# Kernel optimization log

Hardware: AMD Instinct MI355X
Metric: run time of the kernel (lower is better)

Reference implementation:

```python
import jax, jax.numpy as jnp
import numpy as np

B, C, H, W = 8, 128, 64, 64
CQK = C // 8


def setup_inputs() -> dict:
    key = jax.random.key(0)
    ks = jax.random.split(key, 7)
    scale = 1.0 / np.sqrt(C)
    return {
        "x": jax.random.normal(ks[0], (B, C, H, W), dtype=jnp.float32),
        "wq": jax.random.normal(ks[1], (CQK, C), dtype=jnp.float32) * scale,
        "bq": jax.random.normal(ks[2], (CQK,), dtype=jnp.float32) * 0.01,
        "wk": jax.random.normal(ks[3], (CQK, C), dtype=jnp.float32) * scale,
        "bk": jax.random.normal(ks[4], (CQK,), dtype=jnp.float32) * 0.01,
        "wv": jax.random.normal(ks[5], (C, C), dtype=jnp.float32) * scale,
        "bv": jax.random.normal(ks[6], (C,), dtype=jnp.float32) * 0.01,
    }


def reference(x, wq, bq, wk, bk, wv, bv):
    b, c, h, w = x.shape
    n = h * w
    xf = x.reshape(b, c, n)                                  # [B,C,N]
    # 1x1 convs == channel matmuls
    q = jnp.einsum('oc,bcn->bon', wq, xf) + bq[:, None]      # [B,C/8,N]
    k = jnp.einsum('oc,bcn->bon', wk, xf) + bk[:, None]      # [B,C/8,N]
    v = jnp.einsum('oc,bcn->bon', wv, xf) + bv[:, None]      # [B,C,N]
    # energy[b,i,j] = <q[:,i], k[:,j]>  (note: NO 1/sqrt(d) scale, per source)
    energy = jnp.einsum('bci,bcj->bij', q, k)                # [B,N,N]
    att = jax.nn.softmax(energy, axis=-1)                    # softmax over j
    # out[b,c,i] = sum_j v[b,c,j] * att[b,i,j]
    out = jnp.einsum('bcj,bij->bci', v, att).reshape(b, c, h, w)
    return out + x
```

## Files before the change

### kernel.cpp

```cpp
#include <hip/hip_runtime.h>
#include <math.h>

#define NB  8
#define NC  128
#define NN  4096
#define NCQ 16
#define BI  64
#define BJ  64
#define NT  (NN / BJ)
#define WROWS 160

typedef __attribute__((ext_vector_type(8))) short short8v;
typedef __attribute__((ext_vector_type(4))) short short4v;
typedef __attribute__((ext_vector_type(4))) float f32x4;

__device__ __forceinline__ short f2bf(float f) {
    unsigned u = __builtin_bit_cast(unsigned, f);
    u += 0x7fffu + ((u >> 16) & 1u);
    return (short)(u >> 16);
}
__device__ __forceinline__ float bf2f(short h) {
    return __builtin_bit_cast(float, ((unsigned)(unsigned short)h) << 16);
}

__global__ __launch_bounds__(256) void wconv(
    const float* __restrict__ wq, const float* __restrict__ bq,
    const float* __restrict__ wk, const float* __restrict__ bk,
    const float* __restrict__ wv, const float* __restrict__ bv,
    short* __restrict__ whg, short* __restrict__ wlg, float* __restrict__ biasg)
{
    const int idx = blockIdx.x * 256 + threadIdx.x;
    if (idx < WROWS * NC) {
        const int row = idx >> 7, k = idx & 127;
        const float v = (row < 16) ? wq[row * NC + k]
                       : (row < 32) ? wk[(row - 16) * NC + k]
                                    : wv[(row - 32) * NC + k];
        const short h = f2bf(v);
        whg[idx] = h;
        wlg[idx] = f2bf(v - bf2f(h));
    }
    if (idx < WROWS)
        biasg[idx] = (idx < 16) ? bq[idx] : (idx < 32) ? bk[idx - 16] : bv[idx - 32];
}

__global__ __launch_bounds__(256) void qkv_gemm(
    const float* __restrict__ x,
    const short* __restrict__ whg, const short* __restrict__ wlg,
    const float* __restrict__ biasg,
    short* __restrict__ Qo, short* __restrict__ KoT, short* __restrict__ Vo)
{
    __shared__ __align__(16) short xsT[2][64][136];

    const int b  = blockIdx.y;
    const int n0 = blockIdx.x * 64;
    const int t  = threadIdx.x;
    const int w  = t >> 6;
    const int l  = t & 63;
    const int lr = l & 15;
    const int g  = l >> 4;

    const float* xb = x + (size_t)b * NC * NN;

#pragma unroll
    for (int it = 0; it < 8; ++it) {
        const int idx4 = t + 256 * it;
        const int cr = idx4 >> 4;
        const int j4 = (idx4 & 15) * 4;
        const float4 v = *reinterpret_cast<const float4*>(xb + (size_t)cr * NN + n0 + j4);
        const float vf[4] = {v.x, v.y, v.z, v.w};
#pragma unroll
        for (int p = 0; p < 4; ++p) {
            const short h = f2bf(vf[p]);
            xsT[0][j4 + p][cr] = h;
            xsT[1][j4 + p][cr] = f2bf(vf[p] - bf2f(h));
        }
    }
    __syncthreads();

    const int lc = 16 * w + lr;
    f32x4 acc[10];
#pragma unroll
    for (int rt = 0; rt < 10; ++rt) acc[rt] = {0.f, 0.f, 0.f, 0.f};

#pragma unroll
    for (int ks = 0; ks < 4; ++ks) {
        const short8v xh = *reinterpret_cast<const short8v*>(&xsT[0][lc][32 * ks + 8 * g]);
        const short8v xl = *reinterpret_cast<const short8v*>(&xsT[1][lc][32 * ks + 8 * g]);
#pragma unroll
        for (int rt = 0; rt < 10; ++rt) {
            const int wo = (16 * rt + lr) * NC + 32 * ks + 8 * g;
            const short8v ah = *reinterpret_cast<const short8v*>(whg + wo);
            const short8v al = *reinterpret_cast<const short8v*>(wlg + wo);
            acc[rt] = __builtin_amdgcn_mfma_f32_16x16x32_bf16(ah, xh, acc[rt], 0, 0, 0);
            acc[rt] = __builtin_amdgcn_mfma_f32_16x16x32_bf16(ah, xl, acc[rt], 0, 0, 0);
            acc[rt] = __builtin_amdgcn_mfma_f32_16x16x32_bf16(al, xh, acc[rt], 0, 0, 0);
        }
    }

    const int col = n0 + lc;
#pragma unroll
    for (int rt = 0; rt < 10; ++rt) {
#pragma unroll
        for (int r = 0; r < 4; ++r) {
            const int ch = 16 * rt + 4 * g + r;
            const short o = f2bf(acc[rt][r] + biasg[ch]);
            if (rt == 0)
                Qo[((size_t)b * NCQ + ch) * NN + col] = o;
            else if (rt == 1)
                KoT[((size_t)b * NN + col) * NCQ + (ch - 16)] = o;
            else
                Vo[((size_t)b * NC + (ch - 32)) * NN + col] = o;
        }
    }
}

__global__ __launch_bounds__(256) void attn_mfma(
    const short* __restrict__ Q, const short* __restrict__ KT,
    const short* __restrict__ V, const float* __restrict__ x,
    float* __restrict__ out)
{
    __shared__ __align__(16) short psT[2][64][72];
    __shared__ float lsumX[4][4][16];

    const int b  = blockIdx.y;
    const int i0 = blockIdx.x * BI;
    const int t  = threadIdx.x;
    const int w  = t >> 6;
    const int l  = t & 63;
    const int lr = l & 15;
    const int g  = l >> 4;

    const short* Qb  = Q  + (size_t)b * NCQ * NN;
    const short* KTb = KT + (size_t)b * NN * NCQ;
    const short* Vb  = V  + (size_t)b * NC * NN;

    const short8v kzero = {0, 0, 0, 0, 0, 0, 0, 0};
    const f32x4   fzero = {0.f, 0.f, 0.f, 0.f};

    short8v qf[4] = {kzero, kzero, kzero, kzero};
    if (g < 2) {
#pragma unroll
        for (int it = 0; it < 4; ++it) {
            const short* qp = Qb + (size_t)(8 * g) * NN + i0 + 16 * it + lr;
#pragma unroll
            for (int e = 0; e < 8; ++e) qf[it][e] = qp[(size_t)e * NN];
        }
    }

    short8v kfA = kzero;
    if (g < 2)
        kfA = *reinterpret_cast<const short8v*>(KTb + (size_t)(16 * w + lr) * NCQ + 8 * g);

    f32x4 acc[2][4];
#pragma unroll
    for (int ct = 0; ct < 2; ++ct)
#pragma unroll
        for (int it = 0; it < 4; ++it) acc[ct][it] = fzero;
    float lsum[4] = {0.f, 0.f, 0.f, 0.f};

    for (int jt = 0; jt < NT; ++jt) {
        const int cur = jt & 1;

        short8v kfB = kzero;
        if (jt + 1 < NT && g < 2)
            kfB = *reinterpret_cast<const short8v*>(
                    KTb + (size_t)((jt + 1) * BJ + 16 * w + lr) * NCQ + 8 * g);

        short8v vf00, vf01, vf10, vf11;
        if (jt > 0) {
            const short* vp = Vb + (size_t)(32 * w + lr) * NN + (jt - 1) * BJ + 8 * g;
            vf00 = *reinterpret_cast<const short8v*>(vp);
            vf01 = *reinterpret_cast<const short8v*>(vp + 32);
            vf10 = *reinterpret_cast<const short8v*>(vp + 16 * NN);
            vf11 = *reinterpret_cast<const short8v*>(vp + 16 * NN + 32);
        }

        f32x4 e0 = __builtin_amdgcn_mfma_f32_16x16x32_bf16(kfA, qf[0], fzero, 0, 0, 0);
        f32x4 e1 = __builtin_amdgcn_mfma_f32_16x16x32_bf16(kfA, qf[1], fzero, 0, 0, 0);
        f32x4 e2 = __builtin_amdgcn_mfma_f32_16x16x32_bf16(kfA, qf[2], fzero, 0, 0, 0);
        f32x4 e3 = __builtin_amdgcn_mfma_f32_16x16x32_bf16(kfA, qf[3], fzero, 0, 0, 0);

#pragma unroll
        for (int r = 0; r < 4; ++r) e0[r] = __expf(e0[r]);
#pragma unroll
        for (int r = 0; r < 4; ++r) e1[r] = __expf(e1[r]);
#pragma unroll
        for (int r = 0; r < 4; ++r) e2[r] = __expf(e2[r]);
#pragma unroll
        for (int r = 0; r < 4; ++r) e3[r] = __expf(e3[r]);
        lsum[0] += (e0[0] + e0[1]) + (e0[2] + e0[3]);
        lsum[1] += (e1[0] + e1[1]) + (e1[2] + e1[3]);
        lsum[2] += (e2[0] + e2[1]) + (e2[2] + e2[3]);
        lsum[3] += (e3[0] + e3[1]) + (e3[2] + e3[3]);

        if (jt > 0) {
            const int prev = cur ^ 1;
            __builtin_amdgcn_s_setprio(1);
#pragma unroll
            for (int ks = 0; ks < 2; ++ks) {
#pragma unroll
                for (int it = 0; it < 4; ++it) {
                    const short8v pf = *reinterpret_cast<const short8v*>(
                            &psT[prev][16 * it + lr][32 * ks + 8 * g]);
                    acc[0][it] = __builtin_amdgcn_mfma_f32_16x16x32_bf16(
                            ks ? vf01 : vf00, pf, acc[0][it], 0, 0, 0);
                    acc[1][it] = __builtin_amdgcn_mfma_f32_16x16x32_bf16(
                            ks ? vf11 : vf10, pf, acc[1][it], 0, 0, 0);
                }
            }
            __builtin_amdgcn_s_setprio(0);
        }

#define P_STORE(ET, IT)                                                           \
        {                                                                         \
            unsigned p01 = (unsigned short)f2bf(ET[0]) |                          \
                           ((unsigned)(unsigned short)f2bf(ET[1]) << 16);         \
            unsigned p23 = (unsigned short)f2bf(ET[2]) |                          \
                           ((unsigned)(unsigned short)f2bf(ET[3]) << 16);         \
            *reinterpret_cast<unsigned*>(&psT[cur][16 * (IT) + lr][16 * w + 4 * g])     = p01; \
            *reinterpret_cast<unsigned*>(&psT[cur][16 * (IT) + lr][16 * w + 4 * g + 2]) = p23; \
        }
        P_STORE(e0, 0) P_STORE(e1, 1) P_STORE(e2, 2) P_STORE(e3, 3)
#undef P_STORE

        __syncthreads();
        kfA = kfB;
    }

    {
        const int prev = (NT - 1) & 1;
        const short* vp = Vb + (size_t)(32 * w + lr) * NN + (NT - 1) * BJ + 8 * g;
        const short8v vf00 = *reinterpret_cast<const short8v*>(vp);
        const short8v vf01 = *reinterpret_cast<const short8v*>(vp + 32);
        const short8v vf10 = *reinterpret_cast<const short8v*>(vp + 16 * NN);
        const short8v vf11 = *reinterpret_cast<const short8v*>(vp + 16 * NN + 32);
#pragma unroll
        for (int ks = 0; ks < 2; ++ks) {
#pragma unroll
            for (int it = 0; it < 4; ++it) {
                const short8v pf = *reinterpret_cast<const short8v*>(
                        &psT[prev][16 * it + lr][32 * ks + 8 * g]);
                acc[0][it] = __builtin_amdgcn_mfma_f32_16x16x32_bf16(
                        ks ? vf01 : vf00, pf, acc[0][it], 0, 0, 0);
                acc[1][it] = __builtin_amdgcn_mfma_f32_16x16x32_bf16(
                        ks ? vf11 : vf10, pf, acc[1][it], 0, 0, 0);
            }
        }
    }

#pragma unroll
    for (int it = 0; it < 4; ++it) {
        lsum[it] += __shfl_xor(lsum[it], 16);
        lsum[it] += __shfl_xor(lsum[it], 32);
    }
    if (l < 16) {
#pragma unroll
        for (int it = 0; it < 4; ++it) lsumX[w][it][l] = lsum[it];
    }
    __syncthreads();
    float inv[4];
#pragma unroll
    for (int it = 0; it < 4; ++it) {
        const float lr_tot = (lsumX[0][it][lr] + lsumX[1][it][lr]) +
                             (lsumX[2][it][lr] + lsumX[3][it][lr]);
        inv[it] = 1.f / lr_tot;
    }

#pragma unroll
    for (int ct = 0; ct < 2; ++ct) {
#pragma unroll
        for (int it = 0; it < 4; ++it) {
#pragma unroll
            for (int r = 0; r < 4; ++r) {
                const int c = 32 * w + 16 * ct + 4 * g + r;
                const size_t o = ((size_t)b * NC + c) * NN + i0 + 16 * it + lr;
                out[o] = acc[ct][it][r] * inv[it] + x[o];
            }
        }
    }
}

extern "C" void kernel_launch(void* const* d_in, const int* in_sizes, int n_in,
                              void* d_out, int out_size, void* d_ws, size_t ws_size,
                              hipStream_t stream) {
    const float* x  = (const float*)d_in[0];
    const float* wq = (const float*)d_in[1];
    const float* bq = (const float*)d_in[2];
    const float* wk = (const float*)d_in[3];
    const float* bk = (const float*)d_in[4];
    const float* wv = (const float*)d_in[5];
    const float* bv = (const float*)d_in[6];
    float* out = (float*)d_out;

    short* ws = (short*)d_ws;
    short* Qo  = ws;
    short* KoT = ws + (size_t)NB * NCQ * NN;
    short* Vo  = ws + 2 * (size_t)NB * NCQ * NN;
    short* whg = ws + 10 * (size_t)NB * NCQ * NN;
    short* wlg = whg + WROWS * NC;
    float* biasg = (float*)(wlg + WROWS * NC);

    wconv<<<dim3(80), 256, 0, stream>>>(wq, bq, wk, bk, wv, bv, whg, wlg, biasg);
    qkv_gemm<<<dim3(NN / 64, NB), 256, 0, stream>>>(x, whg, wlg, biasg, Qo, KoT, Vo);
    attn_mfma<<<dim3(NN / BI, NB), 256, 0, stream>>>(Qo, KoT, Vo, x, out);
}
```

Baseline: 174.6 us.

## Prefetch V tile one iteration ahead with register ping-pong and packed bf16 convert

The attention loop is unrolled by two, alternating between two register sets for K and V fragments. V for tile jt is now loaded during iteration jt and consumed in jt+1, instead of being loaded right before use, so global-memory latency is hidden behind a full iteration. The manual f2bf rounding is replaced by the v_cvt_pk_bf16_f32 instruction, and the tail PV MFMAs get raised priority. This costs extra VGPRs for the double-buffered V fragments, which may reduce occupancy.

```diff
diff --git a/kernel.cpp b/kernel.cpp
--- a/kernel.cpp
+++ b/kernel.cpp
@@ -147,10 +147,13 @@
         }
     }
 
-    short8v kfA = kzero;
+    short8v kfA = kzero, kfB = kzero;
     if (g < 2)
         kfA = *reinterpret_cast<const short8v*>(KTb + (size_t)(16 * w + lr) * NCQ + 8 * g);
 
+    short8v vfE0 = kzero, vfE1 = kzero, vfE2 = kzero, vfE3 = kzero;
+    short8v vfO0 = kzero, vfO1 = kzero, vfO2 = kzero, vfO3 = kzero;
+
     f32x4 acc[2][4];
 #pragma unroll
     for (int ct = 0; ct < 2; ++ct)
@@ -158,94 +161,91 @@
         for (int it = 0; it < 4; ++it) acc[ct][it] = fzero;
     float lsum[4] = {0.f, 0.f, 0.f, 0.f};
 
-    for (int jt = 0; jt < NT; ++jt) {
-        const int cur = jt & 1;
-
-        short8v kfB = kzero;
-        if (jt + 1 < NT && g < 2)
-            kfB = *reinterpret_cast<const short8v*>(
-                    KTb + (size_t)((jt + 1) * BJ + 16 * w + lr) * NCQ + 8 * g);
-
-        short8v vf00, vf01, vf10, vf11;
-        if (jt > 0) {
-            const short* vp = Vb + (size_t)(32 * w + lr) * NN + (jt - 1) * BJ + 8 * g;
-            vf00 = *reinterpret_cast<const short8v*>(vp);
-            vf01 = *reinterpret_cast<const short8v*>(vp + 32);
-            vf10 = *reinterpret_cast<const short8v*>(vp + 16 * NN);
-            vf11 = *reinterpret_cast<const short8v*>(vp + 16 * NN + 32);
-        }
-
-        f32x4 e0 = __builtin_amdgcn_mfma_f32_16x16x32_bf16(kfA, qf[0], fzero, 0, 0, 0);
-        f32x4 e1 = __builtin_amdgcn_mfma_f32_16x16x32_bf16(kfA, qf[1], fzero, 0, 0, 0);
-        f32x4 e2 = __builtin_amdgcn_mfma_f32_16x16x32_bf16(kfA, qf[2], fzero, 0, 0, 0);
-        f32x4 e3 = __builtin_amdgcn_mfma_f32_16x16x32_bf16(kfA, qf[3], fzero, 0, 0, 0);
-
-#pragma unroll
-        for (int r = 0; r < 4; ++r) e0[r] = __expf(e0[r]);
-#pragma unroll
-        for (int r = 0; r < 4; ++r) e1[r] = __expf(e1[r]);
-#pragma unroll
-        for (int r = 0; r < 4; ++r) e2[r] = __expf(e2[r]);
-#pragma unroll
-        for (int r = 0; r < 4; ++r) e3[r] = __expf(e3[r]);
-        lsum[0] += (e0[0] + e0[1]) + (e0[2] + e0[3]);
-        lsum[1] += (e1[0] + e1[1]) + (e1[2] + e1[3]);
-        lsum[2] += (e2[0] + e2[1]) + (e2[2] + e2[3]);
-        lsum[3] += (e3[0] + e3[1]) + (e3[2] + e3[3]);
-
-        if (jt > 0) {
-            const int prev = cur ^ 1;
-            __builtin_amdgcn_s_setprio(1);
-#pragma unroll
-            for (int ks = 0; ks < 2; ++ks) {
-#pragma unroll
-                for (int it = 0; it < 4; ++it) {
-                    const short8v pf = *reinterpret_cast<const short8v*>(
-                            &psT[prev][16 * it + lr][32 * ks + 8 * g]);
-                    acc[0][it] = __builtin_amdgcn_mfma_f32_16x16x32_bf16(
-                            ks ? vf01 : vf00, pf, acc[0][it], 0, 0, 0);
-                    acc[1][it] = __builtin_amdgcn_mfma_f32_16x16x32_bf16(
-                            ks ? vf11 : vf10, pf, acc[1][it], 0, 0, 0);
-                }
-            }
-            __builtin_amdgcn_s_setprio(0);
-        }
-
-#define P_STORE(ET, IT)                                                           \
+#define ATTN_ITER(JT, CUR, KUSE, KLOAD, VU0, VU1, VU2, VU3, VL0, VL1, VL2, VL3)   \
+    {                                                                             \
+        if ((JT) + 1 < NT && g < 2)                                               \
+            KLOAD = *reinterpret_cast<const short8v*>(                            \
+                    KTb + (size_t)(((JT) + 1) * BJ + 16 * w + lr) * NCQ + 8 * g); \
         {                                                                         \
-            unsigned p01 = (unsigned short)f2bf(ET[0]) |                          \
-                           ((unsigned)(unsigned short)f2bf(ET[1]) << 16);         \
-            unsigned p23 = (unsigned short)f2bf(ET[2]) |                          \
-                           ((unsigned)(unsigned short)f2bf(ET[3]) << 16);         \
-            *reinterpret_cast<unsigned*>(&psT[cur][16 * (IT) + lr][16 * w + 4 * g])     = p01; \
-            *reinterpret_cast<unsigned*>(&psT[cur][16 * (IT) + lr][16 * w + 4 * g + 2]) = p23; \
-        }
-        P_STORE(e0, 0) P_STORE(e1, 1) P_STORE(e2, 2) P_STORE(e3, 3)
-#undef P_STORE
-
-        __syncthreads();
-        kfA = kfB;
-    }
+            const short* vp = Vb + (size_t)(32 * w + lr) * NN + (JT) * BJ + 8 * g;\
+            VL0 = *reinterpret_cast<const short8v*>(vp);                          \
+            VL1 = *reinterpret_cast<const short8v*>(vp + 32);                     \
+            VL2 = *reinterpret_cast<const short8v*>(vp + 16 * NN);                \
+            VL3 = *reinterpret_cast<const short8v*>(vp + 16 * NN + 32);           \
+        }                                                                         \
+        f32x4 e0 = __builtin_amdgcn_mfma_f32_16x16x32_bf16(KUSE, qf[0], fzero, 0, 0, 0); \
+        f32x4 e1 = __builtin_amdgcn_mfma_f32_16x16x32_bf16(KUSE, qf[1], fzero, 0, 0, 0); \
+        f32x4 e2 = __builtin_amdgcn_mfma_f32_16x16x32_bf16(KUSE, qf[2], fzero, 0, 0, 0); \
+        f32x4 e3 = __builtin_amdgcn_mfma_f32_16x16x32_bf16(KUSE, qf[3], fzero, 0, 0, 0); \
+        _Pragma("unroll")                                                         \
+        for (int r = 0; r < 4; ++r) e0[r] = __expf(e0[r]);                        \
+        _Pragma("unroll")                                                         \
+        for (int r = 0; r < 4; ++r) e1[r] = __expf(e1[r]);                        \
+        _Pragma("unroll")                                                         \
+        for (int r = 0; r < 4; ++r) e2[r] = __expf(e2[r]);                        \
+        _Pragma("unroll")                                                         \
+        for (int r = 0; r < 4; ++r) e3[r] = __expf(e3[r]);                        \
+        lsum[0] += (e0[0] + e0[1]) + (e0[2] + e0[3]);                             \
+        lsum[1] += (e1[0] + e1[1]) + (e1[2] + e1[3]);                             \
+        lsum[2] += (e2[0] + e2[1]) + (e2[2] + e2[3]);                             \
+        lsum[3] += (e3[0] + e3[1]) + (e3[2] + e3[3]);                             \
+        if ((JT) > 0) {                                                           \
+            __builtin_amdgcn_s_setprio(1);                                        \
+            _Pragma("unroll")                                                     \
+            for (int ks = 0; ks < 2; ++ks) {                                      \
+                _Pragma("unroll")                                                 \
+                for (int it = 0; it < 4; ++it) {                                  \
+                    const short8v pf = *reinterpret_cast<const short8v*>(         \
+                            &psT[(CUR) ^ 1][16 * it + lr][32 * ks + 8 * g]);      \
+                    acc[0][it] = __builtin_amdgcn_mfma_f32_16x16x32_bf16(         \
+                            ks ? VU1 : VU0, pf, acc[0][it], 0, 0, 0);             \
+                    acc[1][it] = __builtin_amdgcn_mfma_f32_16x16x32_bf16(         \
+                            ks ? VU3 : VU2, pf, acc[1][it], 0, 0, 0);             \
+                }                                                                 \
+            }                                                                     \
+            __builtin_amdgcn_s_setprio(0);                                        \
+        }                                                                         \
+        {                                                                         \
+            unsigned p01, p23;                                                    \
+            _Pragma("unroll")                                                     \
+            for (int it2 = 0; it2 < 4; ++it2) {                                   \
+                const f32x4& ee = (it2 == 0) ? e0 : (it2 == 1) ? e1               \
+                                 : (it2 == 2) ? e2 : e3;                          \
+                asm("v_cvt_pk_bf16_f32 %0, %1, %2"                                \
+                    : "=v"(p01) : "v"(ee[0]), "v"(ee[1]));                        \
+                asm("v_cvt_pk_bf16_f32 %0, %1, %2"                                \
+                    : "=v"(p23) : "v"(ee[2]), "v"(ee[3]));                        \
+                *reinterpret_cast<unsigned*>(                                     \
+                        &psT[CUR][16 * it2 + lr][16 * w + 4 * g])     = p01;      \
+                *reinterpret_cast<unsigned*>(                                     \
+                        &psT[CUR][16 * it2 + lr][16 * w + 4 * g + 2]) = p23;      \
+            }                                                                     \
+        }                                                                         \
+        __syncthreads();                                                          \
+    }
+
+#pragma unroll 1
+    for (int jt2 = 0; jt2 < NT; jt2 += 2) {
+        ATTN_ITER(jt2,     0, kfA, kfB, vfO0, vfO1, vfO2, vfO3, vfE0, vfE1, vfE2, vfE3)
+        ATTN_ITER(jt2 + 1, 1, kfB, kfA, vfE0, vfE1, vfE2, vfE3, vfO0, vfO1, vfO2, vfO3)
+    }
+#undef ATTN_ITER
 
     {
-        const int prev = (NT - 1) & 1;
-        const short* vp = Vb + (size_t)(32 * w + lr) * NN + (NT - 1) * BJ + 8 * g;
-        const short8v vf00 = *reinterpret_cast<const short8v*>(vp);
-        const short8v vf01 = *reinterpret_cast<const short8v*>(vp + 32);
-        const short8v vf10 = *reinterpret_cast<const short8v*>(vp + 16 * NN);
-        const short8v vf11 = *reinterpret_cast<const short8v*>(vp + 16 * NN + 32);
+        __builtin_amdgcn_s_setprio(1);
 #pragma unroll
         for (int ks = 0; ks < 2; ++ks) {
 #pragma unroll
             for (int it = 0; it < 4; ++it) {
                 const short8v pf = *reinterpret_cast<const short8v*>(
-                        &psT[prev][16 * it + lr][32 * ks + 8 * g]);
+                        &psT[1][16 * it + lr][32 * ks + 8 * g]);
                 acc[0][it] = __builtin_amdgcn_mfma_f32_16x16x32_bf16(
-                        ks ? vf01 : vf00, pf, acc[0][it], 0, 0, 0);
+                        ks ? vfO1 : vfO0, pf, acc[0][it], 0, 0, 0);
                 acc[1][it] = __builtin_amdgcn_mfma_f32_16x16x32_bf16(
-                        ks ? vf11 : vf10, pf, acc[1][it], 0, 0, 0);
+                        ks ? vfO3 : vfO2, pf, acc[1][it], 0, 0, 0);
             }
         }
+        __builtin_amdgcn_s_setprio(0);
     }
 
 #pragma unroll
```

Result: faster. 166.7 us (-4.5%).
